# Optimization experiments

Hardware: AMD Instinct MI355X
Metric: run time of the kernel (lower is better)

## Reference

```python
import jax, jax.numpy as jnp
import numpy as np

BN_EPS = 1e-4  # matches torch.nn.BatchNorm1d(eps=0.0001)

def setup_inputs() -> dict:
    key = jax.random.key(0)
    ks = jax.random.split(key, 8)
    N, T, D_in, D_out = 512, 64, 1024, 1024
    return {
        "input_feature_st": jax.random.randint(ks[0], (N, T, D_in), 0, 2).astype(jnp.float32),
        "input_features_sc": jax.random.normal(ks[1], (N, D_in), dtype=jnp.float32),
        "weight": jax.random.normal(ks[2], (D_out, D_in), dtype=jnp.float32) * 0.03,
        "bias": jax.random.normal(ks[3], (D_out,), dtype=jnp.float32) * 0.1,
        "gamma": jax.random.normal(ks[4], (D_out,), dtype=jnp.float32) * 2.0,  # nn.init.normal_(bn.weight, 0, 2.0)
        "beta": jnp.zeros((D_out,), dtype=jnp.float32),
        "running_mean": jax.random.normal(ks[5], (D_out,), dtype=jnp.float32) * 0.1,
        "running_var": jax.random.uniform(ks[6], (D_out,), dtype=jnp.float32, minval=0.5, maxval=1.5),
    }

def _if_scan(pot_in, bias_step):
    # pot_in: (N, T, D_out); bias_step: (D_out,) -> spikes (N, T, D_out)
    pot0 = jnp.zeros(pot_in.shape[::2], dtype=pot_in.dtype)  # (N, D_out)
    def step(pot, p_t):
        pot = pot + p_t + bias_step
        spk = (pot >= 1.0).astype(pot.dtype)
        return pot - spk, spk
    _, spikes_t = jax.lax.scan(step, pot0, jnp.swapaxes(pot_in, 0, 1))  # (T, N, D)
    return jnp.swapaxes(spikes_t, 0, 1)

def reference(input_feature_st, input_features_sc, weight, bias, gamma, beta, running_mean, running_var):
    T = input_feature_st.shape[1]
    # ANN path: Linear + BN (eval stats) + ReLU
    lin = input_features_sc @ weight.T + bias                      # (N, D_out)
    out_bn = gamma * (lin - running_mean) / jnp.sqrt(running_var + BN_EPS) + beta
    ann_output = jax.nn.relu(out_bn)
    # Fold BN into weights for the SNN path (note: no eps, as in source)
    ratio = gamma / jnp.sqrt(running_var)
    w_norm = weight * ratio[:, None]                               # (D_out, D_in)
    b_norm = (bias - running_mean) * ratio + beta                  # (D_out,)
    # Integrate-and-fire scan over T
    pot_in = jnp.einsum("ntd,od->nto", input_feature_st, w_norm)  # (N, T, D_out)
    spike_out = _if_scan(pot_in, b_norm / T)
    spike_count_out = jnp.sum(spike_out, axis=1)                   # (N, D_out)
    return spike_out, spike_count_out
```

## Files before the change

### kernel.cpp

```cpp
#include <hip/hip_runtime.h>
#include <hip/hip_bf16.h>

typedef float  float4v __attribute__((ext_vector_type(4)));
typedef short  short8v __attribute__((ext_vector_type(8)));
typedef short  short4v __attribute__((ext_vector_type(4)));
typedef __bf16 bf16x8  __attribute__((ext_vector_type(8)));
typedef float  f32x4   __attribute__((ext_vector_type(4)));

constexpr int NB = 512, T = 64, DIN = 1024, DOUT = 1024;
constexpr int BM = 128, BN = 128, BK = 64;

constexpr size_t ABF_BYTES = (size_t)NB * T * DIN * 2;
constexpr size_t WN_BYTES  = (size_t)DOUT * DIN * 2;
constexpr size_t WS_BF16   = ABF_BYTES + WN_BYTES;

__device__ __forceinline__ short f2bf_rne(float x) {
    return __builtin_bit_cast(short, __float2bfloat16(x));
}
__device__ __forceinline__ short f2bf_trunc(float x) {
    return (short)(__builtin_bit_cast(unsigned int, x) >> 16);
}
__device__ __forceinline__ void load_lds_16B(const void* g, void* l) {
    __builtin_amdgcn_global_load_lds(
        (const __attribute__((address_space(1))) unsigned int*)g,
        (__attribute__((address_space(3))) unsigned int*)l, 16, 0, 0);
}

__global__ void __launch_bounds__(256)
prep_a_kernel(const float* __restrict__ A, short* __restrict__ Abf) {
    int idx = blockIdx.x * 256 + threadIdx.x;
    const float4v* p = (const float4v*)A + (size_t)idx * 2;
    float4v v0 = __builtin_nontemporal_load(p);
    float4v v1 = __builtin_nontemporal_load(p + 1);
    short8v s;
    #pragma unroll
    for (int j = 0; j < 4; j++) {
        s[j]     = f2bf_trunc(v0[j]);
        s[j + 4] = f2bf_trunc(v1[j]);
    }
    *((short8v*)Abf + idx) = s;
}

__global__ void __launch_bounds__(256)
fold_w_kernel(const float* __restrict__ W, const float* __restrict__ gamma,
              const float* __restrict__ rvar, short* __restrict__ Wn) {
    int idx = blockIdx.x * 256 + threadIdx.x;
    int o = idx >> 8;
    float r = gamma[o] / sqrtf(rvar[o]);
    float4v w = ((const float4v*)W)[idx];
    short4v s;
    #pragma unroll
    for (int j = 0; j < 4; j++) s[j] = f2bf_rne(w[j] * r);
    ((short4v*)Wn)[idx] = s;
}

__global__ void __launch_bounds__(256, 4)
snn_gemm_if_dma(const short* __restrict__ Abf,
                const short* __restrict__ Wn,
                const float* __restrict__ bias, const float* __restrict__ gamma,
                const float* __restrict__ beta, const float* __restrict__ rmean,
                const float* __restrict__ rvar, float* __restrict__ out) {
    __shared__ __align__(16) char smem[32768];
    __shared__ float bstepS[BN];
    char* AsS   = smem;
    char* BsS   = smem + 16384;
    float* potS = (float*)smem;

    const int tid = threadIdx.x;
    const int bs  = blockIdx.x;
    const int oB  = blockIdx.y * BN;

    if (tid < BN) {
        int o = oB + tid;
        float r = gamma[o] / sqrtf(rvar[o]);
        bstepS[tid] = ((bias[o] - rmean[o]) * r + beta[o]) * (1.0f / 64.0f);
    }

    const int lane = tid & 63;
    const int wv   = tid >> 6;
    const int wr   = wv & 1;
    const int wc   = wv >> 1;
    const int l15  = lane & 15;
    const int quad = lane >> 4;

    int srcOff[4];
    #pragma unroll
    for (int i = 0; i < 4; i++) {
        int s   = i * 256 + tid;
        int row = s >> 3;
        int ck  = (s & 7) ^ (row & 7);
        srcOff[i] = (row * DIN + ck * 8) * 2;
    }
    int aOff[4][2], bOff[4][2];
    #pragma unroll
    for (int i = 0; i < 4; i++) {
        int ra = wr * 64 + i * 16 + l15;
        int rb = wc * 64 + i * 16 + l15;
        #pragma unroll
        for (int ks = 0; ks < 2; ks++) {
            int c = ks * 4 + quad;
            aOff[i][ks] = (ra * 8 + (c ^ (ra & 7))) * 16;
            bOff[i][ks] = (rb * 8 + (c ^ (rb & 7))) * 16;
        }
    }

    f32x4 acc[4][4] = {};
    const char* Ab = (const char*)(Abf + (size_t)bs * BM * DIN);
    const char* Bb = (const char*)(Wn + (size_t)oB * DIN);

    for (int kb = 0; kb < DIN; kb += BK) {
        __syncthreads();
        const int kbB = kb * 2;
        #pragma unroll
        for (int i = 0; i < 4; i++) {
            int s = i * 256 + tid;
            load_lds_16B(Ab + srcOff[i] + kbB, AsS + s * 16);
            load_lds_16B(Bb + srcOff[i] + kbB, BsS + s * 16);
        }
        __syncthreads();

        #pragma unroll
        for (int ks = 0; ks < 2; ks++) {
            bf16x8 af[4], bf[4];
            #pragma unroll
            for (int i = 0; i < 4; i++)
                af[i] = __builtin_bit_cast(bf16x8, *(const short8v*)(AsS + aOff[i][ks]));
            #pragma unroll
            for (int i = 0; i < 4; i++)
                bf[i] = __builtin_bit_cast(bf16x8, *(const short8v*)(BsS + bOff[i][ks]));
            #pragma unroll
            for (int mi = 0; mi < 4; mi++)
                #pragma unroll
                for (int ni = 0; ni < 4; ni++)
                    acc[mi][ni] = __builtin_amdgcn_mfma_f32_16x16x32_bf16(
                        af[mi], bf[ni], acc[mi][ni], 0, 0, 0);
        }
    }

    __syncthreads();

    #pragma unroll 1
    for (int s = 0; s < 2; s++) {
        if (wr == s) {
            #pragma unroll
            for (int mi = 0; mi < 4; mi++)
                #pragma unroll
                for (int ni = 0; ni < 4; ni++)
                    #pragma unroll
                    for (int r = 0; r < 4; r++) {
                        int row = mi * 16 + quad * 4 + r;
                        int col = (wc * 64 + ni * 16 + l15) ^ (quad << 3);
                        potS[row * BN + col] = acc[mi][ni][r];
                    }
        }
        __syncthreads();
        if (tid < BN) {
            int n = bs * 2 + s;
            float pot = 0.f, cnt = 0.f;
            const float bst = bstepS[tid];
            float* so = out + (size_t)n * T * DOUT + oB + tid;
            for (int t = 0; t < T; t++) {
                pot += potS[t * BN + (tid ^ (((t >> 2) & 3) << 3))] + bst;
                float spk = (pot >= 1.0f) ? 1.0f : 0.0f;
                pot -= spk;
                cnt += spk;
                __builtin_nontemporal_store(spk, so + (size_t)t * DOUT);
            }
            __builtin_nontemporal_store(
                cnt, out + (size_t)NB * T * DOUT + (size_t)n * DOUT + oB + tid);
        }
        __syncthreads();
    }
}


constexpr int LDA_F = 72;
constexpr int A_BYTES_F = BM * LDA_F * 2;
constexpr int SMEM_F = A_BYTES_F + BN * BK * 2;

template <bool PREFOLD>
__global__ void __launch_bounds__(256)
snn_gemm_if(const float* __restrict__ A, const float* __restrict__ W,
            const short* __restrict__ Wn,
            const float* __restrict__ bias, const float* __restrict__ gamma,
            const float* __restrict__ beta, const float* __restrict__ rmean,
            const float* __restrict__ rvar, float* __restrict__ out) {
    __shared__ __align__(16) char smem[SMEM_F];
    __shared__ float ratioS[BN];
    __shared__ float bstepS[BN];
    short* AsS  = (short*)smem;
    short* BsS  = (short*)(smem + A_BYTES_F);
    float* potS = (float*)smem;

    const int tid   = threadIdx.x;
    const int by    = blockIdx.y;
    const int oBase = blockIdx.x * BN;

    if (tid < BN) {
        int o = oBase + tid;
        float r = gamma[o] / sqrtf(rvar[o]);
        ratioS[tid] = r;
        bstepS[tid] = ((bias[o] - rmean[o]) * r + beta[o]) * (1.0f / 64.0f);
    }
    __syncthreads();

    const int lane = tid & 63;
    const int wv   = tid >> 6;
    const int wr   = wv & 1;
    const int wc   = wv >> 1;
    const int l15  = lane & 15;
    const int quad = lane >> 4;

    f32x4 acc[4][4] = {};
    const float* Ab = A + (size_t)by * BM * DIN;

    for (int kb = 0; kb < DIN; kb += BK) {
        float4v av[4][2];
        #pragma unroll
        for (int i = 0; i < 4; i++) {
            int g = i * 256 + tid;
            int r = g >> 3, k8 = g & 7;
            const float4v* p = (const float4v*)(Ab + (size_t)r * DIN + kb + k8 * 8);
            av[i][0] = p[0];
            av[i][1] = p[1];
        }
        float4v bv[4][2];
        if constexpr (!PREFOLD) {
            #pragma unroll
            for (int i = 0; i < 4; i++) {
                int slot = i * 256 + tid;
                int r = slot >> 3, k8 = (slot & 7) ^ (r & 7);
                const float4v* p = (const float4v*)(W + (size_t)(oBase + r) * DIN + kb + k8 * 8);
                bv[i][0] = p[0];
                bv[i][1] = p[1];
            }
        }
        __syncthreads();

        if constexpr (PREFOLD) {
            #pragma unroll
            for (int i = 0; i < 4; i++) {
                int slot = i * 256 + tid;
                int r = slot >> 3, k8 = (slot & 7) ^ (r & 7);
                load_lds_16B(Wn + (size_t)(oBase + r) * DIN + kb + k8 * 8,
                             BsS + (size_t)slot * 8);
            }
        } else {
            #pragma unroll
            for (int i = 0; i < 4; i++) {
                int slot = i * 256 + tid;
                int r = slot >> 3;
                float rt = ratioS[r];
                short8v s;
                #pragma unroll
                for (int j = 0; j < 4; j++) {
                    s[j]     = f2bf_rne(bv[i][0][j] * rt);
                    s[j + 4] = f2bf_rne(bv[i][1][j] * rt);
                }
                *(short8v*)(BsS + (size_t)slot * 8) = s;
            }
        }
        #pragma unroll
        for (int i = 0; i < 4; i++) {
            int g = i * 256 + tid;
            int r = g >> 3, k8 = g & 7;
            short8v s;
            #pragma unroll
            for (int j = 0; j < 4; j++) {
                s[j]     = f2bf_trunc(av[i][0][j]);
                s[j + 4] = f2bf_trunc(av[i][1][j]);
            }
            *(short8v*)(&AsS[r * LDA_F + k8 * 8]) = s;
        }
        __syncthreads();

        #pragma unroll
        for (int ks = 0; ks < 2; ks++) {
            bf16x8 af[4], bfv[4];
            #pragma unroll
            for (int mi = 0; mi < 4; mi++)
                af[mi] = __builtin_bit_cast(bf16x8,
                    *(const short8v*)(&AsS[(wr * 64 + mi * 16 + l15) * LDA_F + ks * 32 + quad * 8]));
            #pragma unroll
            for (int ni = 0; ni < 4; ni++) {
                int row  = wc * 64 + ni * 16 + l15;
                int slot = row * 8 + ((ks * 4 + quad) ^ (l15 & 7));
                bfv[ni] = __builtin_bit_cast(bf16x8, *(const short8v*)(BsS + (size_t)slot * 8));
            }
            #pragma unroll
            for (int mi = 0; mi < 4; mi++)
                #pragma unroll
                for (int ni = 0; ni < 4; ni++)
                    acc[mi][ni] = __builtin_amdgcn_mfma_f32_16x16x32_bf16(
                        af[mi], bfv[ni], acc[mi][ni], 0, 0, 0);
        }
    }

    __syncthreads();

    #pragma unroll 1
    for (int s = 0; s < 2; s++) {
        if (wr == s) {
            #pragma unroll
            for (int mi = 0; mi < 4; mi++)
                #pragma unroll
                for (int ni = 0; ni < 4; ni++)
                    #pragma unroll
                    for (int r = 0; r < 4; r++)
                        potS[(mi * 16 + quad * 4 + r) * BN + wc * 64 + ni * 16 + l15] =
                            acc[mi][ni][r];
        }
        __syncthreads();
        if (tid < BN) {
            int n = by * 2 + s;
            float pot = 0.f, cnt = 0.f;
            const float bst = bstepS[tid];
            float* so = out + (size_t)n * T * DOUT + oBase + tid;
            for (int t = 0; t < T; t++) {
                pot += potS[t * BN + tid] + bst;
                float spk = (pot >= 1.0f) ? 1.0f : 0.0f;
                pot -= spk;
                cnt += spk;
                so[(size_t)t * DOUT] = spk;
            }
            out[(size_t)NB * T * DOUT + (size_t)n * DOUT + oBase + tid] = cnt;
        }
        __syncthreads();
    }
}

extern "C" void kernel_launch(void* const* d_in, const int* in_sizes, int n_in,
                              void* d_out, int out_size, void* d_ws, size_t ws_size,
                              hipStream_t stream) {
    const float* A     = (const float*)d_in[0];
    const float* W     = (const float*)d_in[2];
    const float* bias  = (const float*)d_in[3];
    const float* gamma = (const float*)d_in[4];
    const float* beta  = (const float*)d_in[5];
    const float* rmean = (const float*)d_in[6];
    const float* rvar  = (const float*)d_in[7];
    float* out = (float*)d_out;

    if (d_ws != nullptr && ws_size >= WS_BF16) {
        short* Abf = (short*)d_ws;
        short* Wn  = (short*)((char*)d_ws + ABF_BYTES);
        prep_a_kernel<<<(NB * T * DIN) / 8 / 256, 256, 0, stream>>>(A, Abf);
        fold_w_kernel<<<DOUT * DIN / 4 / 256, 256, 0, stream>>>(W, gamma, rvar, Wn);
        dim3 grid(NB / 2, DOUT / BN);
        snn_gemm_if_dma<<<grid, 256, 0, stream>>>(Abf, Wn, bias, gamma, beta,
                                                  rmean, rvar, out);
    } else if (d_ws != nullptr && ws_size >= WN_BYTES) {
        short* Wn = (short*)d_ws;
        fold_w_kernel<<<DOUT * DIN / 4 / 256, 256, 0, stream>>>(W, gamma, rvar, Wn);
        dim3 grid(DOUT / BN, NB / 2);
        snn_gemm_if<true><<<grid, 256, 0, stream>>>(A, W, Wn, bias, gamma, beta,
                                                    rmean, rvar, out);
    } else {
        dim3 grid(DOUT / BN, NB / 2);
        snn_gemm_if<false><<<grid, 256, 0, stream>>>(A, W, nullptr, bias, gamma, beta,
                                                     rmean, rvar, out);
    }
}
```

Before: 306.2 us.

## Widen GEMM tile to 128x256 and switch to 32x32x16 MFMA

The block tile grows from 128x128 to 128x256 output columns, so each loaded A tile is reused across twice as many weight columns. The inner product now uses 32x32x16 bf16 MFMA with 2x4 accumulator tiles per wave instead of 16x16x32 with 4x4. The epilogue is reworked into two passes per sample to fit the 128-wide potential buffer, adding extra barriers. LDS rises to 48KB and launch bounds drop to 2 blocks per CU, which lowers occupancy and halves the grid along the output dimension.

New measurement: 320.4 us. +4.6%, slower.

```diff
diff --git a/kernel.cpp b/kernel.cpp
--- a/kernel.cpp
+++ b/kernel.cpp
@@ -6,9 +6,11 @@
 typedef short  short4v __attribute__((ext_vector_type(4)));
 typedef __bf16 bf16x8  __attribute__((ext_vector_type(8)));
 typedef float  f32x4   __attribute__((ext_vector_type(4)));
+typedef float  f32x16  __attribute__((ext_vector_type(16)));
 
 constexpr int NB = 512, T = 64, DIN = 1024, DOUT = 1024;
 constexpr int BM = 128, BN = 128, BK = 64;
+constexpr int BN2 = 256;
 
 constexpr size_t ABF_BYTES = (size_t)NB * T * DIN * 2;
 constexpr size_t WN_BYTES  = (size_t)DOUT * DIN * 2;
@@ -54,23 +56,23 @@
     ((short4v*)Wn)[idx] = s;
 }
 
-__global__ void __launch_bounds__(256, 4)
-snn_gemm_if_dma(const short* __restrict__ Abf,
-                const short* __restrict__ Wn,
-                const float* __restrict__ bias, const float* __restrict__ gamma,
-                const float* __restrict__ beta, const float* __restrict__ rmean,
-                const float* __restrict__ rvar, float* __restrict__ out) {
-    __shared__ __align__(16) char smem[32768];
-    __shared__ float bstepS[BN];
+__global__ void __launch_bounds__(256, 2)
+snn_gemm_if_dma2(const short* __restrict__ Abf,
+                 const short* __restrict__ Wn,
+                 const float* __restrict__ bias, const float* __restrict__ gamma,
+                 const float* __restrict__ beta, const float* __restrict__ rmean,
+                 const float* __restrict__ rvar, float* __restrict__ out) {
+    __shared__ __align__(16) char smem[49152];
+    __shared__ float bstepS[BN2];
     char* AsS   = smem;
     char* BsS   = smem + 16384;
     float* potS = (float*)smem;
 
     const int tid = threadIdx.x;
     const int bs  = blockIdx.x;
-    const int oB  = blockIdx.y * BN;
-
-    if (tid < BN) {
+    const int oB  = blockIdx.y * BN2;
+
+    {
         int o = oB + tid;
         float r = gamma[o] / sqrtf(rvar[o]);
         bstepS[tid] = ((bias[o] - rmean[o]) * r + beta[o]) * (1.0f / 64.0f);
@@ -80,31 +82,30 @@
     const int wv   = tid >> 6;
     const int wr   = wv & 1;
     const int wc   = wv >> 1;
-    const int l15  = lane & 15;
-    const int quad = lane >> 4;
-
-    int srcOff[4];
+    const int l31  = lane & 31;
+    const int half = lane >> 5;
+    const int s7   = lane & 7;
+
+    int srcA[4], srcB[8];
     #pragma unroll
     for (int i = 0; i < 4; i++) {
-        int s   = i * 256 + tid;
-        int row = s >> 3;
-        int ck  = (s & 7) ^ (row & 7);
-        srcOff[i] = (row * DIN + ck * 8) * 2;
-    }
-    int aOff[4][2], bOff[4][2];
-    #pragma unroll
-    for (int i = 0; i < 4; i++) {
-        int ra = wr * 64 + i * 16 + l15;
-        int rb = wc * 64 + i * 16 + l15;
-        #pragma unroll
-        for (int ks = 0; ks < 2; ks++) {
-            int c = ks * 4 + quad;
-            aOff[i][ks] = (ra * 8 + (c ^ (ra & 7))) * 16;
-            bOff[i][ks] = (rb * 8 + (c ^ (rb & 7))) * 16;
-        }
-    }
-
-    f32x4 acc[4][4] = {};
+        int s = i * 256 + tid, row = s >> 3, ck = (s & 7) ^ (row & 7);
+        srcA[i] = row * (DIN * 2) + ck * 16;
+    }
+    #pragma unroll
+    for (int i = 0; i < 8; i++) {
+        int s = i * 256 + tid, row = s >> 3, ck = (s & 7) ^ (row & 7);
+        srcB[i] = row * (DIN * 2) + ck * 16;
+    }
+    int baseA[2], baseB[4], cx[4];
+    #pragma unroll
+    for (int mi = 0; mi < 2; mi++) baseA[mi] = (wr * 64 + mi * 32 + l31) * 128;
+    #pragma unroll
+    for (int ni = 0; ni < 4; ni++) baseB[ni] = (wc * 128 + ni * 32 + l31) * 128;
+    #pragma unroll
+    for (int ks = 0; ks < 4; ks++) cx[ks] = ((ks * 2 + half) ^ s7) * 16;
+
+    f32x16 acc[2][4] = {};
     const char* Ab = (const char*)(Abf + (size_t)bs * BM * DIN);
     const char* Bb = (const char*)(Wn + (size_t)oB * DIN);
 
@@ -112,27 +113,29 @@
         __syncthreads();
         const int kbB = kb * 2;
         #pragma unroll
-        for (int i = 0; i < 4; i++) {
-            int s = i * 256 + tid;
-            load_lds_16B(Ab + srcOff[i] + kbB, AsS + s * 16);
-            load_lds_16B(Bb + srcOff[i] + kbB, BsS + s * 16);
-        }
-        __syncthreads();
-
-        #pragma unroll
-        for (int ks = 0; ks < 2; ks++) {
-            bf16x8 af[4], bf[4];
-            #pragma unroll
-            for (int i = 0; i < 4; i++)
-                af[i] = __builtin_bit_cast(bf16x8, *(const short8v*)(AsS + aOff[i][ks]));
-            #pragma unroll
-            for (int i = 0; i < 4; i++)
-                bf[i] = __builtin_bit_cast(bf16x8, *(const short8v*)(BsS + bOff[i][ks]));
-            #pragma unroll
-            for (int mi = 0; mi < 4; mi++)
+        for (int i = 0; i < 4; i++)
+            load_lds_16B(Ab + srcA[i] + kbB, AsS + (i * 256 + tid) * 16);
+        #pragma unroll
+        for (int i = 0; i < 8; i++)
+            load_lds_16B(Bb + srcB[i] + kbB, BsS + (i * 256 + tid) * 16);
+        __syncthreads();
+
+        #pragma unroll
+        for (int ks = 0; ks < 4; ks++) {
+            bf16x8 af[2], bf[4];
+            #pragma unroll
+            for (int mi = 0; mi < 2; mi++)
+                af[mi] = __builtin_bit_cast(bf16x8,
+                    *(const short8v*)(AsS + baseA[mi] + cx[ks]));
+            #pragma unroll
+            for (int ni = 0; ni < 4; ni++)
+                bf[ni] = __builtin_bit_cast(bf16x8,
+                    *(const short8v*)(BsS + baseB[ni] + cx[ks]));
+            #pragma unroll
+            for (int mi = 0; mi < 2; mi++)
                 #pragma unroll
                 for (int ni = 0; ni < 4; ni++)
-                    acc[mi][ni] = __builtin_amdgcn_mfma_f32_16x16x32_bf16(
+                    acc[mi][ni] = __builtin_amdgcn_mfma_f32_32x32x16_bf16(
                         af[mi], bf[ni], acc[mi][ni], 0, 0, 0);
         }
     }
@@ -141,35 +144,37 @@
 
     #pragma unroll 1
     for (int s = 0; s < 2; s++) {
-        if (wr == s) {
-            #pragma unroll
-            for (int mi = 0; mi < 4; mi++)
-                #pragma unroll
-                for (int ni = 0; ni < 4; ni++)
+        #pragma unroll 1
+        for (int h = 0; h < 2; h++) {
+            if (wr == s && wc == h) {
+                #pragma unroll
+                for (int mi = 0; mi < 2; mi++)
                     #pragma unroll
-                    for (int r = 0; r < 4; r++) {
-                        int row = mi * 16 + quad * 4 + r;
-                        int col = (wc * 64 + ni * 16 + l15) ^ (quad << 3);
-                        potS[row * BN + col] = acc[mi][ni][r];
-                    }
-        }
-        __syncthreads();
-        if (tid < BN) {
-            int n = bs * 2 + s;
-            float pot = 0.f, cnt = 0.f;
-            const float bst = bstepS[tid];
-            float* so = out + (size_t)n * T * DOUT + oB + tid;
-            for (int t = 0; t < T; t++) {
-                pot += potS[t * BN + (tid ^ (((t >> 2) & 3) << 3))] + bst;
-                float spk = (pot >= 1.0f) ? 1.0f : 0.0f;
-                pot -= spk;
-                cnt += spk;
-                __builtin_nontemporal_store(spk, so + (size_t)t * DOUT);
-            }
-            __builtin_nontemporal_store(
-                cnt, out + (size_t)NB * T * DOUT + (size_t)n * DOUT + oB + tid);
-        }
-        __syncthreads();
+                    for (int ni = 0; ni < 4; ni++)
+                        #pragma unroll
+                        for (int reg = 0; reg < 16; reg++) {
+                            int t = mi * 32 + (reg & 3) + 8 * (reg >> 2) + 4 * half;
+                            potS[t * 128 + ni * 32 + l31] = acc[mi][ni][reg];
+                        }
+            }
+            __syncthreads();
+            if (tid < 128) {
+                int n = bs * 2 + s;
+                float pot = 0.f, cnt = 0.f;
+                const float bst = bstepS[h * 128 + tid];
+                float* so = out + (size_t)n * T * DOUT + oB + h * 128 + tid;
+                for (int t = 0; t < T; t++) {
+                    pot += potS[t * 128 + tid] + bst;
+                    float spk = (pot >= 1.0f) ? 1.0f : 0.0f;
+                    pot -= spk;
+                    cnt += spk;
+                    __builtin_nontemporal_store(spk, so + (size_t)t * DOUT);
+                }
+                __builtin_nontemporal_store(
+                    cnt, out + (size_t)NB * T * DOUT + (size_t)n * DOUT + oB + h * 128 + tid);
+            }
+            __syncthreads();
+        }
     }
 }
 
@@ -346,9 +351,9 @@
         short* Wn  = (short*)((char*)d_ws + ABF_BYTES);
         prep_a_kernel<<<(NB * T * DIN) / 8 / 256, 256, 0, stream>>>(A, Abf);
         fold_w_kernel<<<DOUT * DIN / 4 / 256, 256, 0, stream>>>(W, gamma, rvar, Wn);
-        dim3 grid(NB / 2, DOUT / BN);
-        snn_gemm_if_dma<<<grid, 256, 0, stream>>>(Abf, Wn, bias, gamma, beta,
-                                                  rmean, rvar, out);
+        dim3 grid(NB / 2, DOUT / BN2);
+        snn_gemm_if_dma2<<<grid, 256, 0, stream>>>(Abf, Wn, bias, gamma, beta,
+                                                   rmean, rvar, out);
     } else if (d_ws != nullptr && ws_size >= WN_BYTES) {
         short* Wn = (short*)d_ws;
         fold_w_kernel<<<DOUT * DIN / 4 / 256, 256, 0, stream>>>(W, gamma, rvar, Wn);
```

## Load weight fragments directly from global into registers, swap grid order

Applied to the files above, without the earlier changes.

The B (folded weight) operand no longer goes through LDS. Each lane loads its MFMA B fragments straight from global memory into registers, so only the A tile is staged through LDS. The grid is transposed so consecutive blocks share the same A rows across output tiles, and launch bounds drop to 3 waves per SIMD to make room for the extra registers. This removes LDS writes and reads for B but trades them for uncoalesced, per-lane 16-byte global loads with no prefetch overlap, plus higher register pressure.

New measurement: 372.4 us. +21.6%, slower.

```diff
diff --git a/kernel.cpp b/kernel.cpp
--- a/kernel.cpp
+++ b/kernel.cpp
@@ -54,21 +54,20 @@
     ((short4v*)Wn)[idx] = s;
 }
 
-__global__ void __launch_bounds__(256, 4)
-snn_gemm_if_dma(const short* __restrict__ Abf,
-                const short* __restrict__ Wn,
-                const float* __restrict__ bias, const float* __restrict__ gamma,
-                const float* __restrict__ beta, const float* __restrict__ rmean,
-                const float* __restrict__ rvar, float* __restrict__ out) {
+__global__ void __launch_bounds__(256, 3)
+snn_gemm_if_bdir(const short* __restrict__ Abf,
+                 const short* __restrict__ Wn,
+                 const float* __restrict__ bias, const float* __restrict__ gamma,
+                 const float* __restrict__ beta, const float* __restrict__ rmean,
+                 const float* __restrict__ rvar, float* __restrict__ out) {
     __shared__ __align__(16) char smem[32768];
     __shared__ float bstepS[BN];
     char* AsS   = smem;
-    char* BsS   = smem + 16384;
     float* potS = (float*)smem;
 
     const int tid = threadIdx.x;
-    const int bs  = blockIdx.x;
-    const int oB  = blockIdx.y * BN;
+    const int oB  = blockIdx.x * BN;
+    const int bs  = blockIdx.y;
 
     if (tid < BN) {
         int o = oB + tid;
@@ -83,57 +82,53 @@
     const int l15  = lane & 15;
     const int quad = lane >> 4;
 
-    int srcOff[4];
+    int srcA[4];
     #pragma unroll
     for (int i = 0; i < 4; i++) {
-        int s   = i * 256 + tid;
-        int row = s >> 3;
-        int ck  = (s & 7) ^ (row & 7);
-        srcOff[i] = (row * DIN + ck * 8) * 2;
-    }
-    int aOff[4][2], bOff[4][2];
+        int s = i * 256 + tid, row = s >> 3, ck = (s & 7) ^ (row & 7);
+        srcA[i] = row * (DIN * 2) + ck * 16;
+    }
+    int aOff[4][2];
     #pragma unroll
     for (int i = 0; i < 4; i++) {
         int ra = wr * 64 + i * 16 + l15;
-        int rb = wc * 64 + i * 16 + l15;
         #pragma unroll
         for (int ks = 0; ks < 2; ks++) {
             int c = ks * 4 + quad;
             aOff[i][ks] = (ra * 8 + (c ^ (ra & 7))) * 16;
-            bOff[i][ks] = (rb * 8 + (c ^ (rb & 7))) * 16;
-        }
-    }
+        }
+    }
+    const short* Bl = Wn + (size_t)(oB + wc * 64 + l15) * DIN + quad * 8;
 
     f32x4 acc[4][4] = {};
     const char* Ab = (const char*)(Abf + (size_t)bs * BM * DIN);
-    const char* Bb = (const char*)(Wn + (size_t)oB * DIN);
 
     for (int kb = 0; kb < DIN; kb += BK) {
         __syncthreads();
-        const int kbB = kb * 2;
-        #pragma unroll
-        for (int i = 0; i < 4; i++) {
-            int s = i * 256 + tid;
-            load_lds_16B(Ab + srcOff[i] + kbB, AsS + s * 16);
-            load_lds_16B(Bb + srcOff[i] + kbB, BsS + s * 16);
-        }
+        #pragma unroll
+        for (int i = 0; i < 4; i++)
+            load_lds_16B(Ab + srcA[i] + kb * 2, AsS + (i * 256 + tid) * 16);
+        short8v bfr[2][4];
+        #pragma unroll
+        for (int ks = 0; ks < 2; ks++)
+            #pragma unroll
+            for (int ni = 0; ni < 4; ni++)
+                bfr[ks][ni] = *(const short8v*)(Bl + (size_t)ni * 16 * DIN + kb + ks * 32);
         __syncthreads();
 
         #pragma unroll
         for (int ks = 0; ks < 2; ks++) {
-            bf16x8 af[4], bf[4];
-            #pragma unroll
-            for (int i = 0; i < 4; i++)
-                af[i] = __builtin_bit_cast(bf16x8, *(const short8v*)(AsS + aOff[i][ks]));
-            #pragma unroll
-            for (int i = 0; i < 4; i++)
-                bf[i] = __builtin_bit_cast(bf16x8, *(const short8v*)(BsS + bOff[i][ks]));
+            bf16x8 af[4];
+            #pragma unroll
+            for (int mi = 0; mi < 4; mi++)
+                af[mi] = __builtin_bit_cast(bf16x8, *(const short8v*)(AsS + aOff[mi][ks]));
             #pragma unroll
             for (int mi = 0; mi < 4; mi++)
                 #pragma unroll
                 for (int ni = 0; ni < 4; ni++)
                     acc[mi][ni] = __builtin_amdgcn_mfma_f32_16x16x32_bf16(
-                        af[mi], bf[ni], acc[mi][ni], 0, 0, 0);
+                        af[mi], __builtin_bit_cast(bf16x8, bfr[ks][ni]),
+                        acc[mi][ni], 0, 0, 0);
         }
     }
 
@@ -346,9 +341,9 @@
         short* Wn  = (short*)((char*)d_ws + ABF_BYTES);
         prep_a_kernel<<<(NB * T * DIN) / 8 / 256, 256, 0, stream>>>(A, Abf);
         fold_w_kernel<<<DOUT * DIN / 4 / 256, 256, 0, stream>>>(W, gamma, rvar, Wn);
-        dim3 grid(NB / 2, DOUT / BN);
-        snn_gemm_if_dma<<<grid, 256, 0, stream>>>(Abf, Wn, bias, gamma, beta,
-                                                  rmean, rvar, out);
+        dim3 grid(DOUT / BN, NB / 2);
+        snn_gemm_if_bdir<<<grid, 256, 0, stream>>>(Abf, Wn, bias, gamma, beta,
+                                                   rmean, rvar, out);
     } else if (d_ws != nullptr && ws_size >= WN_BYTES) {
         short* Wn = (short*)d_ws;
         fold_w_kernel<<<DOUT * DIN / 4 / 256, 256, 0, stream>>>(W, gamma, rvar, Wn);
```
